# Performance work log

Measured on AMD Instinct MI355X. Metric: run time of the kernel, lower is better.

## Reference

```python
import jax, jax.numpy as jnp
import numpy as np

N_NODES = 100000
N_EDGES = 1600000
N_FEAT = 64
HIDDEN = 64
N_GRAPHS = 256
BN_EPS = 1e-5


def gcn_conv(x, src, dst, edge_weight, W, b):
    # PyG GCNConv with normalize=False: linear transform, then weighted scatter-add.
    h = x @ W                                   # [N, H]
    msgs = edge_weight[:, None] * h[src]        # [E, H] gather + scale
    agg = jax.ops.segment_sum(msgs, dst, num_segments=N_NODES)  # scatter-add
    return agg + b


def setup_inputs() -> dict:
    key = jax.random.key(0)
    ks = jax.random.split(key, 12)
    x = jax.random.normal(ks[0], (N_NODES, N_FEAT), dtype=jnp.float32)
    edge_index = jax.random.randint(ks[1], (2, N_EDGES), 0, N_NODES, dtype=jnp.int64)
    edge_weight = jax.random.uniform(ks[2], (N_EDGES,), dtype=jnp.float32)
    batch = jnp.sort(jax.random.randint(ks[3], (N_NODES,), 0, N_GRAPHS, dtype=jnp.int64))
    s1 = 1.0 / np.sqrt(N_FEAT)
    s2 = 1.0 / np.sqrt(HIDDEN)
    W1 = jax.random.uniform(ks[4], (N_FEAT, HIDDEN), minval=-s1, maxval=s1)
    b1 = jnp.zeros((HIDDEN,), jnp.float32)
    W2 = jax.random.uniform(ks[5], (HIDDEN, HIDDEN), minval=-s2, maxval=s2)
    b2 = jnp.zeros((HIDDEN,), jnp.float32)
    W3 = jax.random.uniform(ks[6], (HIDDEN, HIDDEN), minval=-s2, maxval=s2)
    b3 = jnp.zeros((HIDDEN,), jnp.float32)
    gamma = jnp.ones((HIDDEN,), jnp.float32)
    beta = jnp.zeros((HIDDEN,), jnp.float32)
    linW = jax.random.uniform(ks[7], (HIDDEN, 1), minval=-s2, maxval=s2)
    linb = jnp.zeros((1,), jnp.float32)
    return {"x": x, "edge_index": edge_index, "edge_weight": edge_weight,
            "batch": batch, "W1": W1, "b1": b1, "W2": W2, "b2": b2,
            "W3": W3, "b3": b3, "gamma": gamma, "beta": beta,
            "linW": linW, "linb": linb}


def reference(x, edge_index, edge_weight, batch, W1, b1, W2, b2, W3, b3,
              gamma, beta, linW, linb):
    src, dst = edge_index[0], edge_index[1]
    h = jax.nn.relu(gcn_conv(x, src, dst, edge_weight, W1, b1))
    h = jax.nn.relu(gcn_conv(h, src, dst, edge_weight, W2, b2))
    h = gcn_conv(h, src, dst, edge_weight, W3, b3)
    # global max pool per graph -> [G, H]
    pooled = jax.ops.segment_max(h, batch, num_segments=N_GRAPHS)
    # BatchNorm1d (training mode: batch statistics, biased variance)
    mean = jnp.mean(pooled, axis=0)
    var = jnp.var(pooled, axis=0)
    normed = (pooled - mean) * jax.lax.rsqrt(var + BN_EPS) * gamma + beta
    return normed @ linW + linb  # [G, 1]
```

## Files before the change

kernel.cpp:

```cpp
#include <hip/hip_runtime.h>

#define N_NODES 100000
#define N_EDGES 1600000
#define NGRAPHS 256
#define BN_EPS 1e-5f
#define NBUK ((N_NODES + 511) >> 9)
#define BCAP 8704
#define BIN_EPB 2048
#define BIN_BLOCKS ((N_EDGES + BIN_EPB - 1) / BIN_EPB)
#define POOL_RUN 8


__device__ __forceinline__ unsigned f2ord(float f) {
  unsigned u = __float_as_uint(f);
  return (u & 0x80000000u) ? ~u : (u | 0x80000000u);
}

__device__ __forceinline__ float ord2f(unsigned u) {
  unsigned bits = (u & 0x80000000u) ? (u ^ 0x80000000u) : ~u;
  return __uint_as_float(bits);
}

__device__ __forceinline__ unsigned short f2bf(float f) {
  unsigned u = __float_as_uint(f);
  unsigned r = u + 0x7FFFu + ((u >> 16) & 1u);
  return (unsigned short)(r >> 16);
}

__device__ __forceinline__ float bf2f(unsigned short b) {
  return __uint_as_float(((unsigned)b) << 16);
}

__global__ void detect_init(const unsigned* __restrict__ ei, int* __restrict__ flag,
                            int* __restrict__ cursor) {
  const int tid = threadIdx.x;
  if (tid < NBUK) cursor[tid] = tid * BCAP;
  if (tid == 0) {
    int f = 1;
    for (int i = 1; i < 64; i += 2) {
      if (ei[i] != 0u) { f = 0; break; }
    }
    *flag = f;
  }
}

__global__ void detect_i64(const unsigned* __restrict__ ei, int* __restrict__ flag) {
  if (blockIdx.x == 0 && threadIdx.x == 0) {
    int f = 1;
    for (int i = 1; i < 64; i += 2) {
      if (ei[i] != 0u) { f = 0; break; }
    }
    *flag = f;
  }
}

__device__ __forceinline__ int load_idx(const void* p, const int* flag, long long i) {
  return (*flag) ? (int)((const long long*)p)[i] : ((const int*)p)[i];
}


__global__ __launch_bounds__(256) void binpass(const void* __restrict__ eiPtr,
                                               const int* __restrict__ flag,
                                               const float* __restrict__ ew,
                                               int* __restrict__ cursor,
                                               int2* __restrict__ tmp) {
  __shared__ int cnt[NBUK];
  __shared__ int base[NBUK];
  const int tid = threadIdx.x;
  const long long chunk0 = (long long)blockIdx.x * BIN_EPB;
  for (int i = tid; i < NBUK; i += 256) cnt[i] = 0;
  __syncthreads();
  int pk[8], wb[8], rk[8], bk[8];
  const bool i64 = (*flag != 0);
  #pragma unroll
  for (int j = 0; j < 8; ++j) {
    long long e = chunk0 + j * 256 + tid;
    rk[j] = -1;
    if (e < N_EDGES) {
      int s, d;
      if (i64) {
        const long long* ei = (const long long*)eiPtr;
        s = (int)ei[e]; d = (int)ei[N_EDGES + e];
      } else {
        const int* ei = (const int*)eiPtr;
        s = ei[e]; d = ei[N_EDGES + e];
      }
      wb[j] = __float_as_int(ew[e]);
      bk[j] = d >> 9;
      pk[j] = s | ((d & 511) << 18);
      rk[j] = atomicAdd(&cnt[bk[j]], 1);
    }
  }
  __syncthreads();
  for (int b = tid; b < NBUK; b += 256) {
    int c = cnt[b];
    base[b] = c ? atomicAdd(&cursor[b], c) : 0;
  }
  __syncthreads();
  #pragma unroll
  for (int j = 0; j < 8; ++j) {
    if (rk[j] >= 0) {
      int pos = base[bk[j]] + rk[j];
      if (pos < (bk[j] + 1) * BCAP) {
        int2 r; r.x = pk[j]; r.y = wb[j];
        tmp[pos] = r;
      }
    }
  }
}

__global__ __launch_bounds__(256) void place2(const int2* __restrict__ tmp,
                                              const int* __restrict__ cursor,
                                              int2* __restrict__ rowPtr2,
                                              int2* __restrict__ csrP) {
  __shared__ int cnt[512];
  __shared__ int sc[256];
  __shared__ int cur[512];
  const int b = blockIdx.x;
  const int tid = threadIdx.x;
  const int beg = b * BCAP;
  int cntb = cursor[b] - beg;
  if (cntb > BCAP) cntb = BCAP;
  const int end = beg + cntb;
  cnt[tid] = 0; cnt[tid + 256] = 0;
  __syncthreads();
  for (int i = beg + tid; i < end; i += 256) {
    atomicAdd(&cnt[(tmp[i].x >> 18) & 511], 1);
  }
  __syncthreads();
  int c0 = cnt[2 * tid], c1 = cnt[2 * tid + 1];
  int pairSum = c0 + c1;
  sc[tid] = pairSum;
  __syncthreads();
  for (int off = 1; off < 256; off <<= 1) {
    int t = (tid >= off) ? sc[tid - off] : 0;
    __syncthreads();
    sc[tid] += t;
    __syncthreads();
  }
  int exclPair = sc[tid] - pairSum;
  int base0 = beg + exclPair;
  int base1 = base0 + c0;
  int g0 = (b << 9) + 2 * tid;
  if (g0 < N_NODES)     { int2 r; r.x = base0; r.y = base0 + c0; rowPtr2[g0] = r; }
  if (g0 + 1 < N_NODES) { int2 r; r.x = base1; r.y = base1 + c1; rowPtr2[g0 + 1] = r; }
  cur[2 * tid] = base0;
  cur[2 * tid + 1] = base1;
  __syncthreads();
  for (int i = beg + tid; i < end; i += 256) {
    int2 e = tmp[i];
    int pos = atomicAdd(&cur[(e.x >> 18) & 511], 1);
    int2 r; r.x = e.x & 0x3FFFF; r.y = e.y;
    csrP[pos] = r;
  }
}


template<bool F32IN>
__global__ __launch_bounds__(256) void gemm_u(const void* __restrict__ Ain,
                                              const float* __restrict__ W,
                                              unsigned short* __restrict__ Uout,
                                              int N) {
  __shared__ float Wt[64][68];
  __shared__ float At[64][68];
  const int tid = threadIdx.x;
  const int rowBase = blockIdx.x * 64;

  for (int i = tid; i < 4096; i += 256) {
    int k = i >> 6, c = i & 63;
    Wt[c][k] = W[i];
  }
  if (F32IN) {
    const float4* A4 = (const float4*)Ain;
    #pragma unroll
    for (int j = 0; j < 4; ++j) {
      int t4 = tid + j * 256;
      int g4 = rowBase * 16 + t4;
      float4 v = make_float4(0.f, 0.f, 0.f, 0.f);
      if (g4 < N * 16) v = A4[g4];
      int r = t4 >> 4, k4 = t4 & 15;
      *(float4*)&At[r][k4 * 4] = v;
    }
  } else {
    const uint4* A16 = (const uint4*)Ain;
    #pragma unroll
    for (int j = 0; j < 2; ++j) {
      int q = tid + j * 256;
      int r = q >> 3, c8 = (q & 7) * 8;
      int grow = rowBase + r;
      uint4 v = make_uint4(0u, 0u, 0u, 0u);
      if (grow < N) v = A16[(size_t)grow * 8 + (q & 7)];
      float4 f0, f1;
      f0.x = bf2f((unsigned short)(v.x & 0xFFFFu)); f0.y = bf2f((unsigned short)(v.x >> 16));
      f0.z = bf2f((unsigned short)(v.y & 0xFFFFu)); f0.w = bf2f((unsigned short)(v.y >> 16));
      f1.x = bf2f((unsigned short)(v.z & 0xFFFFu)); f1.y = bf2f((unsigned short)(v.z >> 16));
      f1.z = bf2f((unsigned short)(v.w & 0xFFFFu)); f1.w = bf2f((unsigned short)(v.w >> 16));
      *(float4*)&At[r][c8] = f0;
      *(float4*)&At[r][c8 + 4] = f1;
    }
  }
  __syncthreads();

  const int c = tid & 63;
  const int r0 = (tid >> 6) * 16;
  float acc[16];
  #pragma unroll
  for (int i = 0; i < 16; ++i) acc[i] = 0.f;

  for (int k0 = 0; k0 < 64; k0 += 4) {
    float4 w = *(const float4*)&Wt[c][k0];
    #pragma unroll
    for (int i = 0; i < 16; ++i) {
      float4 a = *(const float4*)&At[r0 + i][k0];
      acc[i] += a.x * w.x + a.y * w.y + a.z * w.z + a.w * w.w;
    }
  }

  #pragma unroll
  for (int i = 0; i < 16; ++i) {
    int row = rowBase + r0 + i;
    if (row < N) Uout[(size_t)row * 64 + c] = f2bf(acc[i]);
  }
}


__device__ __forceinline__ float2 gather2(const unsigned short* __restrict__ T,
                                          const int2* __restrict__ csr,
                                          int i0, int e0, int i1, int e1, int lane) {
  float a0 = 0.f, a1 = 0.f, b0 = 0.f, b1 = 0.f;
  while ((i0 + 8 <= e0) && (i1 + 8 <= e1)) {
    int2 m0[8], m1[8];
    #pragma unroll
    for (int j = 0; j < 8; ++j) m0[j] = csr[i0 + j];
    #pragma unroll
    for (int j = 0; j < 8; ++j) m1[j] = csr[i1 + j];
    float v0[8], v1[8];
    #pragma unroll
    for (int j = 0; j < 8; ++j) v0[j] = bf2f(T[(size_t)m0[j].x * 64 + lane]);
    #pragma unroll
    for (int j = 0; j < 8; ++j) v1[j] = bf2f(T[(size_t)m1[j].x * 64 + lane]);
    #pragma unroll
    for (int j = 0; j < 8; j += 2) {
      a0 = fmaf(__int_as_float(m0[j].y),     v0[j],     a0);
      a1 = fmaf(__int_as_float(m0[j + 1].y), v0[j + 1], a1);
      b0 = fmaf(__int_as_float(m1[j].y),     v1[j],     b0);
      b1 = fmaf(__int_as_float(m1[j + 1].y), v1[j + 1], b1);
    }
    i0 += 8; i1 += 8;
  }
  while (i0 < e0) {
    const int last = e0 - 1;
    int2 m[8]; float w[8];
    #pragma unroll
    for (int j = 0; j < 8; ++j) {
      int idx = i0 + j;
      int c = idx < last ? idx : last;
      m[j] = csr[c];
      w[j] = (idx < e0) ? __int_as_float(m[j].y) : 0.f;
    }
    float v[8];
    #pragma unroll
    for (int j = 0; j < 8; ++j) v[j] = bf2f(T[(size_t)m[j].x * 64 + lane]);
    #pragma unroll
    for (int j = 0; j < 8; j += 2) {
      a0 = fmaf(w[j],     v[j],     a0);
      a1 = fmaf(w[j + 1], v[j + 1], a1);
    }
    i0 += 8;
  }
  while (i1 < e1) {
    const int last = e1 - 1;
    int2 m[8]; float w[8];
    #pragma unroll
    for (int j = 0; j < 8; ++j) {
      int idx = i1 + j;
      int c = idx < last ? idx : last;
      m[j] = csr[c];
      w[j] = (idx < e1) ? __int_as_float(m[j].y) : 0.f;
    }
    float v[8];
    #pragma unroll
    for (int j = 0; j < 8; ++j) v[j] = bf2f(T[(size_t)m[j].x * 64 + lane]);
    #pragma unroll
    for (int j = 0; j < 8; j += 2) {
      b0 = fmaf(w[j],     v[j],     b0);
      b1 = fmaf(w[j + 1], v[j + 1], b1);
    }
    i1 += 8;
  }
  return make_float2(a0 + a1, b0 + b1);
}


__global__ __launch_bounds__(256) void pull_relu(const unsigned short* __restrict__ T,
                                                 const int2* __restrict__ rowPtr2,
                                                 const int2* __restrict__ csr,
                                                 const float* __restrict__ bias,
                                                 unsigned short* __restrict__ Hout) {
  int wv = __builtin_amdgcn_readfirstlane((blockIdx.x * 256 + threadIdx.x) >> 6);
  const int lane = threadIdx.x & 63;
  const int n0 = wv * 2;
  if (n0 >= N_NODES) return;
  const bool has1 = (n0 + 1 < N_NODES);
  const int2 be0 = rowPtr2[n0];
  const int2 be1 = has1 ? rowPtr2[n0 + 1] : make_int2(0, 0);
  float2 a = gather2(T, csr, be0.x, be0.y, be1.x, be1.y, lane);
  const float bl = bias[lane];
  Hout[(size_t)n0 * 64 + lane] = f2bf(fmaxf(a.x + bl, 0.f));
  if (has1) Hout[(size_t)(n0 + 1) * 64 + lane] = f2bf(fmaxf(a.y + bl, 0.f));
}


__global__ __launch_bounds__(256) void pull_pool(const unsigned short* __restrict__ T,
                                                 const int2* __restrict__ rowPtr2,
                                                 const int2* __restrict__ csr,
                                                 const float* __restrict__ bias,
                                                 const void* __restrict__ bPtr,
                                                 const int* __restrict__ flag,
                                                 unsigned* __restrict__ pooled) {
  int wseq = __builtin_amdgcn_readfirstlane((blockIdx.x * 256 + threadIdx.x) >> 6);
  const int lane = threadIdx.x & 63;
  const int n0 = wseq * POOL_RUN;
  if (n0 >= N_NODES) return;
  const int n1 = min(n0 + POOL_RUN, N_NODES);
  const float blane = bias[lane];
  int curg = load_idx(bPtr, flag, n0);
  float best = -3.4e38f;
  for (int n = n0; n < n1; n += 2) {
    const bool has1 = (n + 1 < n1);
    const int2 be0 = rowPtr2[n];
    const int2 be1 = has1 ? rowPtr2[n + 1] : make_int2(0, 0);
    float2 vv = gather2(T, csr, be0.x, be0.y, be1.x, be1.y, lane);
    float v0 = vv.x + blane;
    int g0 = load_idx(bPtr, flag, n);
    if (g0 != curg) {
      atomicMax(&pooled[curg * 64 + lane], f2ord(best));
      curg = g0; best = v0;
    } else {
      best = fmaxf(best, v0);
    }
    if (has1) {
      float v1 = vv.y + blane;
      int g1 = load_idx(bPtr, flag, n + 1);
      if (g1 != curg) {
        atomicMax(&pooled[curg * 64 + lane], f2ord(best));
        curg = g1; best = v1;
      } else {
        best = fmaxf(best, v1);
      }
    }
  }
  atomicMax(&pooled[curg * 64 + lane], f2ord(best));
}


template<bool RELU_IN, bool ADD_BIAS, bool RELU_OUT>
__global__ __launch_bounds__(256) void gemm64(const float* A,
                                              const float* __restrict__ W,
                                              const float* __restrict__ b,
                                              float* C, int N) {
  __shared__ float Wt[64][68];
  __shared__ float At[64][68];
  const int tid = threadIdx.x;
  const int rowBase = blockIdx.x * 64;

  for (int i = tid; i < 4096; i += 256) {
    int k = i >> 6, c = i & 63;
    Wt[c][k] = W[i];
  }
  const float4* A4 = (const float4*)A;
  #pragma unroll
  for (int j = 0; j < 4; ++j) {
    int t4 = tid + j * 256;
    int g4 = rowBase * 16 + t4;
    float4 v = make_float4(0.f, 0.f, 0.f, 0.f);
    if (g4 < N * 16) v = A4[g4];
    if (RELU_IN) {
      v.x = fmaxf(v.x, 0.f); v.y = fmaxf(v.y, 0.f);
      v.z = fmaxf(v.z, 0.f); v.w = fmaxf(v.w, 0.f);
    }
    int r = t4 >> 4, k4 = t4 & 15;
    *(float4*)&At[r][k4 * 4] = v;
  }
  __syncthreads();

  const int c = tid & 63;
  const int r0 = (tid >> 6) * 16;
  float acc[16];
  #pragma unroll
  for (int i = 0; i < 16; ++i) acc[i] = 0.f;

  for (int k0 = 0; k0 < 64; k0 += 4) {
    float4 w = *(const float4*)&Wt[c][k0];
    #pragma unroll
    for (int i = 0; i < 16; ++i) {
      float4 a = *(const float4*)&At[r0 + i][k0];
      acc[i] += a.x * w.x + a.y * w.y + a.z * w.z + a.w * w.w;
    }
  }

  const float bias = ADD_BIAS ? b[c] : 0.f;
  #pragma unroll
  for (int i = 0; i < 16; ++i) {
    int row = rowBase + r0 + i;
    if (row < N) {
      float v = acc[i] + bias;
      if (RELU_OUT) v = fmaxf(v, 0.f);
      C[row * 64 + c] = v;
    }
  }
}

__global__ __launch_bounds__(256) void init_bias(float* __restrict__ agg,
                                                 const float* __restrict__ b, int n4) {
  int i = blockIdx.x * 256 + threadIdx.x;
  if (i >= n4) return;
  ((float4*)agg)[i] = ((const float4*)b)[i & 15];
}

__global__ __launch_bounds__(256) void scatter_add(const float* __restrict__ h,
                                                   const void* __restrict__ eiPtr,
                                                   const int* __restrict__ flag,
                                                   const float* __restrict__ ew,
                                                   float* __restrict__ agg) {
  int gtid = blockIdx.x * 256 + threadIdx.x;
  int e = gtid >> 6, lane = gtid & 63;
  if (e >= N_EDGES) return;
  int s = load_idx(eiPtr, flag, e);
  int d = load_idx(eiPtr, flag, (long long)N_EDGES + e);
  atomicAdd(&agg[d * 64 + lane], ew[e] * h[s * 64 + lane]);
}

__global__ __launch_bounds__(256) void seg_max(const float* __restrict__ h,
                                               const void* __restrict__ bPtr,
                                               const int* __restrict__ flag,
                                               unsigned* __restrict__ pooled) {
  int gtid = blockIdx.x * 256 + threadIdx.x;
  int n = gtid >> 6, lane = gtid & 63;
  if (n >= N_NODES) return;
  int g = load_idx(bPtr, flag, n);
  atomicMax(&pooled[g * 64 + lane], f2ord(h[n * 64 + lane]));
}


__global__ __launch_bounds__(256) void bn_head(const unsigned* __restrict__ pooled,
                                               const float* __restrict__ gamma,
                                               const float* __restrict__ beta,
                                               const float* __restrict__ linW,
                                               const float* __restrict__ linb,
                                               float* __restrict__ out) {
  __shared__ float P[NGRAPHS][64 + 1];
  __shared__ float mean_s[64], rstd_s[64];
  const int tid = threadIdx.x;

  for (int i = tid; i < NGRAPHS * 64; i += 256) {
    P[i >> 6][i & 63] = ord2f(pooled[i]);
  }
  __syncthreads();

  if (tid < 64) {
    float s = 0.f, ss = 0.f;
    for (int g = 0; g < NGRAPHS; ++g) {
      float v = P[g][tid];
      s += v; ss += v * v;
    }
    float m = s / (float)NGRAPHS;
    float var = ss / (float)NGRAPHS - m * m;
    mean_s[tid] = m;
    rstd_s[tid] = rsqrtf(var + BN_EPS);
  }
  __syncthreads();

  float acc = linb[0];
  #pragma unroll 8
  for (int c = 0; c < 64; ++c) {
    float normed = (P[tid][c] - mean_s[c]) * rstd_s[c] * gamma[c] + beta[c];
    acc += normed * linW[c];
  }
  out[tid] = acc;
}


extern "C" void kernel_launch(void* const* d_in, const int* in_sizes, int n_in,
                              void* d_out, int out_size, void* d_ws, size_t ws_size,
                              hipStream_t stream) {
  const float* x     = (const float*)d_in[0];
  const void*  ei    = d_in[1];
  const float* ew    = (const float*)d_in[2];
  const void*  batch = d_in[3];
  const float* W1    = (const float*)d_in[4];
  const float* b1    = (const float*)d_in[5];
  const float* W2    = (const float*)d_in[6];
  const float* b2    = (const float*)d_in[7];
  const float* W3    = (const float*)d_in[8];
  const float* b3    = (const float*)d_in[9];
  const float* gamma = (const float*)d_in[10];
  const float* beta  = (const float*)d_in[11];
  const float* linW  = (const float*)d_in[12];
  const float* linb  = (const float*)d_in[13];

  char* ws = (char*)d_ws;
  const size_t MAT  = (size_t)N_NODES * 64 * sizeof(float);
  const size_t TBL  = (size_t)N_NODES * 64 * sizeof(unsigned short);
  const size_t CSRP = (size_t)NBUK * BCAP * sizeof(int2);
  const size_t PTR2 = ((size_t)N_NODES * sizeof(int2) + 255) & ~(size_t)255;

  size_t off = 0;
  unsigned short* uA = (unsigned short*)(ws + off); off += TBL;
  unsigned short* hB = (unsigned short*)(ws + off); off += TBL;
  int2*  csrP   = (int2*)(ws + off);           off += CSRP;
  int2*  rowPtr2 = (int2*)(ws + off);          off += PTR2;
  int*   cursor = (int*)(ws + off);            off += 1024;
  unsigned* pooled = (unsigned*)(ws + off);    off += (size_t)NGRAPHS * 64 * sizeof(unsigned);
  int*   flag   = (int*)(ws + off);            off += 256;
  const bool csrPath = (ws_size >= off);

  const int gemmBlocks = (N_NODES + 63) / 64;
  const int nodeWaveBlocks = (N_NODES * 64) / 256;
  const int pairBlocks = (N_NODES / 2 + 3) / 4;
  const int poolBlocks = (N_NODES + POOL_RUN * 4 - 1) / (POOL_RUN * 4);

  if (csrPath) {
    int2* tmpP = (int2*)uA;
    detect_init<<<1, 256, 0, stream>>>((const unsigned*)ei, flag, cursor);
    binpass<<<BIN_BLOCKS, 256, 0, stream>>>(ei, flag, ew, cursor, tmpP);
    place2<<<NBUK, 256, 0, stream>>>(tmpP, cursor, rowPtr2, csrP);

    gemm_u<true><<<gemmBlocks, 256, 0, stream>>>(x, W1, uA, N_NODES);
    pull_relu<<<pairBlocks, 256, 0, stream>>>(uA, rowPtr2, csrP, b1, hB);
    gemm_u<false><<<gemmBlocks, 256, 0, stream>>>(hB, W2, uA, N_NODES);
    pull_relu<<<pairBlocks, 256, 0, stream>>>(uA, rowPtr2, csrP, b2, hB);
    gemm_u<false><<<gemmBlocks, 256, 0, stream>>>(hB, W3, uA, N_NODES);
    hipMemsetAsync(pooled, 0, (size_t)NGRAPHS * 64 * sizeof(unsigned), stream);
    pull_pool<<<poolBlocks, 256, 0, stream>>>(uA, rowPtr2, csrP, b3, batch, flag, pooled);

    bn_head<<<1, 256, 0, stream>>>(pooled, gamma, beta, linW, linb, (float*)d_out);
  } else {
    float* h   = (float*)ws;
    float* agg = (float*)(ws + MAT);
    unsigned* pooled2 = (unsigned*)(ws + 2 * MAT);
    int* flag2 = (int*)(ws + 2 * MAT + (size_t)NGRAPHS * 64 * sizeof(unsigned));
    detect_i64<<<1, 64, 0, stream>>>((const unsigned*)ei, flag2);
    const int n4 = N_NODES * 16;
    const int initBlocks = (n4 + 255) / 256;
    const int scatBlocks = (N_EDGES * 64) / 256;

    gemm64<false, false, false><<<gemmBlocks, 256, 0, stream>>>(x, W1, b1, h, N_NODES);
    init_bias<<<initBlocks, 256, 0, stream>>>(agg, b1, n4);
    scatter_add<<<scatBlocks, 256, 0, stream>>>(h, ei, flag2, ew, agg);
    gemm64<true, false, false><<<gemmBlocks, 256, 0, stream>>>(agg, W2, b2, h, N_NODES);
    init_bias<<<initBlocks, 256, 0, stream>>>(agg, b2, n4);
    scatter_add<<<scatBlocks, 256, 0, stream>>>(h, ei, flag2, ew, agg);
    gemm64<true, false, false><<<gemmBlocks, 256, 0, stream>>>(agg, W3, b3, h, N_NODES);
    init_bias<<<initBlocks, 256, 0, stream>>>(agg, b3, n4);
    scatter_add<<<scatBlocks, 256, 0, stream>>>(h, ei, flag2, ew, agg);

    hipMemsetAsync(pooled2, 0, (size_t)NGRAPHS * 64 * sizeof(unsigned), stream);
    seg_max<<<nodeWaveBlocks, 256, 0, stream>>>(agg, batch, flag2, pooled2);
    bn_head<<<1, 256, 0, stream>>>(pooled2, gamma, beta, linW, linb, (float*)d_out);
  }
}
```

Before: 272.8 us.

## Fuse CSR placement with first GEMM and fold pooled memset into init

```diff
diff --git a/kernel.cpp b/kernel.cpp
--- a/kernel.cpp
+++ b/kernel.cpp
@@ -32,9 +32,10 @@
 }
 
 __global__ void detect_init(const unsigned* __restrict__ ei, int* __restrict__ flag,
-                            int* __restrict__ cursor) {
+                            int* __restrict__ cursor, unsigned* __restrict__ pooled) {
   const int tid = threadIdx.x;
   if (tid < NBUK) cursor[tid] = tid * BCAP;
+  for (int i = tid; i < NGRAPHS * 64; i += 256) pooled[i] = 0u;
   if (tid == 0) {
     int f = 1;
     for (int i = 1; i < 64; i += 2) {
@@ -109,55 +110,98 @@
   }
 }
 
-__global__ __launch_bounds__(256) void place2(const int2* __restrict__ tmp,
-                                              const int* __restrict__ cursor,
-                                              int2* __restrict__ rowPtr2,
-                                              int2* __restrict__ csrP) {
-  __shared__ int cnt[512];
-  __shared__ int sc[256];
-  __shared__ int cur[512];
-  const int b = blockIdx.x;
+
+__global__ __launch_bounds__(256) void place2_gemm1(
+    const int2* __restrict__ tmp, const int* __restrict__ cursor,
+    int2* __restrict__ rowPtr2, int2* __restrict__ csrP,
+    const float* __restrict__ x, const float* __restrict__ W,
+    unsigned short* __restrict__ Uout) {
+  __shared__ float smem[2][64][68];
   const int tid = threadIdx.x;
-  const int beg = b * BCAP;
-  int cntb = cursor[b] - beg;
-  if (cntb > BCAP) cntb = BCAP;
-  const int end = beg + cntb;
-  cnt[tid] = 0; cnt[tid + 256] = 0;
-  __syncthreads();
-  for (int i = beg + tid; i < end; i += 256) {
-    atomicAdd(&cnt[(tmp[i].x >> 18) & 511], 1);
-  }
-  __syncthreads();
-  int c0 = cnt[2 * tid], c1 = cnt[2 * tid + 1];
-  int pairSum = c0 + c1;
-  sc[tid] = pairSum;
-  __syncthreads();
-  for (int off = 1; off < 256; off <<= 1) {
-    int t = (tid >= off) ? sc[tid - off] : 0;
+
+  if (blockIdx.x < NBUK) {
+    int* cnt = (int*)&smem[0][0][0];
+    int* sc  = cnt + 512;
+    int* cur = sc + 256;
+    const int b = blockIdx.x;
+    const int beg = b * BCAP;
+    int cntb = cursor[b] - beg;
+    if (cntb > BCAP) cntb = BCAP;
+    const int end = beg + cntb;
+    cnt[tid] = 0; cnt[tid + 256] = 0;
     __syncthreads();
-    sc[tid] += t;
+    for (int i = beg + tid; i < end; i += 256) {
+      atomicAdd(&cnt[(tmp[i].x >> 18) & 511], 1);
+    }
     __syncthreads();
-  }
-  int exclPair = sc[tid] - pairSum;
-  int base0 = beg + exclPair;
-  int base1 = base0 + c0;
-  int g0 = (b << 9) + 2 * tid;
-  if (g0 < N_NODES)     { int2 r; r.x = base0; r.y = base0 + c0; rowPtr2[g0] = r; }
-  if (g0 + 1 < N_NODES) { int2 r; r.x = base1; r.y = base1 + c1; rowPtr2[g0 + 1] = r; }
-  cur[2 * tid] = base0;
-  cur[2 * tid + 1] = base1;
-  __syncthreads();
-  for (int i = beg + tid; i < end; i += 256) {
-    int2 e = tmp[i];
-    int pos = atomicAdd(&cur[(e.x >> 18) & 511], 1);
-    int2 r; r.x = e.x & 0x3FFFF; r.y = e.y;
-    csrP[pos] = r;
-  }
-}
-
-
-template<bool F32IN>
-__global__ __launch_bounds__(256) void gemm_u(const void* __restrict__ Ain,
+    int c0 = cnt[2 * tid], c1 = cnt[2 * tid + 1];
+    int pairSum = c0 + c1;
+    sc[tid] = pairSum;
+    __syncthreads();
+    for (int off = 1; off < 256; off <<= 1) {
+      int t = (tid >= off) ? sc[tid - off] : 0;
+      __syncthreads();
+      sc[tid] += t;
+      __syncthreads();
+    }
+    int exclPair = sc[tid] - pairSum;
+    int base0 = beg + exclPair;
+    int base1 = base0 + c0;
+    int g0 = (b << 9) + 2 * tid;
+    if (g0 < N_NODES)     { int2 r; r.x = base0; r.y = base0 + c0; rowPtr2[g0] = r; }
+    if (g0 + 1 < N_NODES) { int2 r; r.x = base1; r.y = base1 + c1; rowPtr2[g0 + 1] = r; }
+    cur[2 * tid] = base0;
+    cur[2 * tid + 1] = base1;
+    __syncthreads();
+    for (int i = beg + tid; i < end; i += 256) {
+      int2 e = tmp[i];
+      int pos = atomicAdd(&cur[(e.x >> 18) & 511], 1);
+      int2 r; r.x = e.x & 0x3FFFF; r.y = e.y;
+      csrP[pos] = r;
+    }
+  } else {
+    const int rowBase = (blockIdx.x - NBUK) * 64;
+    float (*Wt)[68] = (float(*)[68])&smem[0][0][0];
+    float (*At)[68] = (float(*)[68])&smem[1][0][0];
+    for (int i = tid; i < 4096; i += 256) {
+      int k = i >> 6, c = i & 63;
+      Wt[c][k] = W[i];
+    }
+    const float4* A4 = (const float4*)x;
+    #pragma unroll
+    for (int j = 0; j < 4; ++j) {
+      int t4 = tid + j * 256;
+      int g4 = rowBase * 16 + t4;
+      float4 v = make_float4(0.f, 0.f, 0.f, 0.f);
+      if (g4 < N_NODES * 16) v = A4[g4];
+      int r = t4 >> 4, k4 = t4 & 15;
+      *(float4*)&At[r][k4 * 4] = v;
+    }
+    __syncthreads();
+
+    const int c = tid & 63;
+    const int r0 = (tid >> 6) * 16;
+    float acc[16];
+    #pragma unroll
+    for (int i = 0; i < 16; ++i) acc[i] = 0.f;
+    for (int k0 = 0; k0 < 64; k0 += 4) {
+      float4 w = *(const float4*)&Wt[c][k0];
+      #pragma unroll
+      for (int i = 0; i < 16; ++i) {
+        float4 a = *(const float4*)&At[r0 + i][k0];
+        acc[i] += a.x * w.x + a.y * w.y + a.z * w.z + a.w * w.w;
+      }
+    }
+    #pragma unroll
+    for (int i = 0; i < 16; ++i) {
+      int row = rowBase + r0 + i;
+      if (row < N_NODES) Uout[(size_t)row * 64 + c] = f2bf(acc[i]);
+    }
+  }
+}
+
+
+__global__ __launch_bounds__(256) void gemm_u(const unsigned short* __restrict__ Ain,
                                               const float* __restrict__ W,
                                               unsigned short* __restrict__ Uout,
                                               int N) {
@@ -170,34 +214,21 @@
     int k = i >> 6, c = i & 63;
     Wt[c][k] = W[i];
   }
-  if (F32IN) {
-    const float4* A4 = (const float4*)Ain;
-    #pragma unroll
-    for (int j = 0; j < 4; ++j) {
-      int t4 = tid + j * 256;
-      int g4 = rowBase * 16 + t4;
-      float4 v = make_float4(0.f, 0.f, 0.f, 0.f);
-      if (g4 < N * 16) v = A4[g4];
-      int r = t4 >> 4, k4 = t4 & 15;
-      *(float4*)&At[r][k4 * 4] = v;
-    }
-  } else {
-    const uint4* A16 = (const uint4*)Ain;
-    #pragma unroll
-    for (int j = 0; j < 2; ++j) {
-      int q = tid + j * 256;
-      int r = q >> 3, c8 = (q & 7) * 8;
-      int grow = rowBase + r;
-      uint4 v = make_uint4(0u, 0u, 0u, 0u);
-      if (grow < N) v = A16[(size_t)grow * 8 + (q & 7)];
-      float4 f0, f1;
-      f0.x = bf2f((unsigned short)(v.x & 0xFFFFu)); f0.y = bf2f((unsigned short)(v.x >> 16));
-      f0.z = bf2f((unsigned short)(v.y & 0xFFFFu)); f0.w = bf2f((unsigned short)(v.y >> 16));
-      f1.x = bf2f((unsigned short)(v.z & 0xFFFFu)); f1.y = bf2f((unsigned short)(v.z >> 16));
-      f1.z = bf2f((unsigned short)(v.w & 0xFFFFu)); f1.w = bf2f((unsigned short)(v.w >> 16));
-      *(float4*)&At[r][c8] = f0;
-      *(float4*)&At[r][c8 + 4] = f1;
-    }
+  const uint4* A16 = (const uint4*)Ain;
+  #pragma unroll
+  for (int j = 0; j < 2; ++j) {
+    int q = tid + j * 256;
+    int r = q >> 3, c8 = (q & 7) * 8;
+    int grow = rowBase + r;
+    uint4 v = make_uint4(0u, 0u, 0u, 0u);
+    if (grow < N) v = A16[(size_t)grow * 8 + (q & 7)];
+    float4 f0, f1;
+    f0.x = bf2f((unsigned short)(v.x & 0xFFFFu)); f0.y = bf2f((unsigned short)(v.x >> 16));
+    f0.z = bf2f((unsigned short)(v.y & 0xFFFFu)); f0.w = bf2f((unsigned short)(v.y >> 16));
+    f1.x = bf2f((unsigned short)(v.z & 0xFFFFu)); f1.y = bf2f((unsigned short)(v.z >> 16));
+    f1.z = bf2f((unsigned short)(v.w & 0xFFFFu)); f1.w = bf2f((unsigned short)(v.w >> 16));
+    *(float4*)&At[r][c8] = f0;
+    *(float4*)&At[r][c8 + 4] = f1;
   }
   __syncthreads();
 
@@ -509,6 +540,7 @@
   unsigned short* uA = (unsigned short*)(ws + off); off += TBL;
   unsigned short* hB = (unsigned short*)(ws + off); off += TBL;
   int2*  csrP   = (int2*)(ws + off);           off += CSRP;
+  int2*  tmpP   = (int2*)(ws + off);           off += CSRP;
   int2*  rowPtr2 = (int2*)(ws + off);          off += PTR2;
   int*   cursor = (int*)(ws + off);            off += 1024;
   unsigned* pooled = (unsigned*)(ws + off);    off += (size_t)NGRAPHS * 64 * sizeof(unsigned);
@@ -521,17 +553,15 @@
   const int poolBlocks = (N_NODES + POOL_RUN * 4 - 1) / (POOL_RUN * 4);
 
   if (csrPath) {
-    int2* tmpP = (int2*)uA;
-    detect_init<<<1, 256, 0, stream>>>((const unsigned*)ei, flag, cursor);
+    detect_init<<<1, 256, 0, stream>>>((const unsigned*)ei, flag, cursor, pooled);
     binpass<<<BIN_BLOCKS, 256, 0, stream>>>(ei, flag, ew, cursor, tmpP);
-    place2<<<NBUK, 256, 0, stream>>>(tmpP, cursor, rowPtr2, csrP);
-
-    gemm_u<true><<<gemmBlocks, 256, 0, stream>>>(x, W1, uA, N_NODES);
+    place2_gemm1<<<NBUK + gemmBlocks, 256, 0, stream>>>(tmpP, cursor, rowPtr2, csrP,
+                                                        x, W1, uA);
+
     pull_relu<<<pairBlocks, 256, 0, stream>>>(uA, rowPtr2, csrP, b1, hB);
-    gemm_u<false><<<gemmBlocks, 256, 0, stream>>>(hB, W2, uA, N_NODES);
+    gemm_u<<<gemmBlocks, 256, 0, stream>>>(hB, W2, uA, N_NODES);
     pull_relu<<<pairBlocks, 256, 0, stream>>>(uA, rowPtr2, csrP, b2, hB);
-    gemm_u<false><<<gemmBlocks, 256, 0, stream>>>(hB, W3, uA, N_NODES);
-    hipMemsetAsync(pooled, 0, (size_t)NGRAPHS * 64 * sizeof(unsigned), stream);
+    gemm_u<<<gemmBlocks, 256, 0, stream>>>(hB, W3, uA, N_NODES);
     pull_pool<<<poolBlocks, 256, 0, stream>>>(uA, rowPtr2, csrP, b3, batch, flag, pooled);
 
     bn_head<<<1, 256, 0, stream>>>(pooled, gamma, beta, linW, linb, (float*)d_out);
```

New measurement: 251.4 us. 1.09x faster.
